# Kernel optimization log

Hardware: AMD Instinct MI355X
Metric: run time of the kernel (lower is better)

The kernel has to match this reference:

```python
import jax, jax.numpy as jnp
import numpy as np

B, T, C = 2, 2048, 1024
H = 16
D = C // H  # head_dim = 64


def setup_inputs() -> dict:
    key = jax.random.key(0)
    k1, k2, k3, k4, k5 = jax.random.split(key, 5)
    s = 0.02
    return {
        "x": jax.random.normal(k1, (B, T, C), dtype=jnp.float32),
        "w_qkv": jax.random.normal(k2, (C, 3 * C), dtype=jnp.float32) * s,
        "b_qkv": jnp.zeros((3 * C,), dtype=jnp.float32),
        "w_proj": jax.random.normal(k3, (C, C), dtype=jnp.float32) * s,
        "b_proj": jnp.zeros((C,), dtype=jnp.float32),
    }


def reference(x, w_qkv, b_qkv, w_proj, b_proj):
    b, t, c = x.shape
    qkv = x @ w_qkv + b_qkv                      # [B,T,3C]
    q, k, v = jnp.split(qkv, 3, axis=-1)
    # [B,T,C] -> [B,H,T,D]
    q = q.reshape(b, t, H, D).transpose(0, 2, 1, 3)
    k = k.reshape(b, t, H, D).transpose(0, 2, 1, 3)
    v = v.reshape(b, t, H, D).transpose(0, 2, 1, 3)
    att = jnp.einsum("bhqd,bhkd->bhqk", q, k) / jnp.sqrt(jnp.float32(D))
    causal = jnp.tril(jnp.ones((t, t), dtype=bool))  # True where allowed
    att = jnp.where(causal, att, -jnp.inf)
    att = jax.nn.softmax(att, axis=-1)
    out = jnp.einsum("bhqk,bhkd->bhqd", att, v)      # [B,H,T,D]
    out = out.transpose(0, 2, 1, 3).reshape(b, t, c)
    return out @ w_proj + b_proj
```

## Files before the change

### kernel.cpp

```cpp
#include <hip/hip_runtime.h>
#include <hip/hip_bf16.h>
#include <math.h>
#include <stdint.h>

#define B_ 2
#define T_ 2048
#define C_ 1024
#define H_ 16
#define D_ 64

typedef __attribute__((ext_vector_type(8))) short bf16x8;
typedef __attribute__((ext_vector_type(4))) float f32x4;

__device__ inline short f2bf(float f) {
  __hip_bfloat16 h = __float2bfloat16(f);
  return *(short*)&h;
}

__device__ inline void async16(const void* g, void* l) {
  __builtin_amdgcn_global_load_lds(
      (const __attribute__((address_space(1))) uint32_t*)g,
      (__attribute__((address_space(3))) uint32_t*)l, 16, 0, 0);
}


__global__ __launch_bounds__(256) void prep(
    const float* __restrict__ X, const float* __restrict__ Wq,
    const float* __restrict__ Wp, short* __restrict__ Xb,
    short* __restrict__ Wqt, short* __restrict__ Wpt) {
  const int tid = threadIdx.x;
  const int blk = blockIdx.x;
  __shared__ short Ts[64][68];

  if (blk < 512) {
    int t = blk * 256 + tid;
    int m = t >> 5, g = t & 31;
    const float* src = X + (size_t)m * C_ + g * 32;
    short* dst = Xb + (size_t)m * C_ + g * 32;
    int xv = (m >> 1) & 3;
    short out[32];
#pragma unroll
    for (int ch = 0; ch < 4; ++ch) {
      int sc = ch ^ xv;
#pragma unroll
      for (int e = 0; e < 8; e += 4) {
        float4 v = *(const float4*)(src + sc * 8 + e);
        out[ch * 8 + e + 0] = f2bf(v.x);
        out[ch * 8 + e + 1] = f2bf(v.y);
        out[ch * 8 + e + 2] = f2bf(v.z);
        out[ch * 8 + e + 3] = f2bf(v.w);
      }
    }
#pragma unroll
    for (int q = 0; q < 4; ++q) *(uint4*)(dst + q * 8) = *(uint4*)(out + q * 8);
    return;
  }

  const float* W;
  short* Wt;
  int N, n0, k0;
  if (blk < 1280) {
    int i = blk - 512;
    W = Wq; Wt = Wqt; N = 3 * C_;
    n0 = (i % 48) * 64; k0 = (i / 48) * 64;
  } else {
    int i = blk - 1280;
    W = Wp; Wt = Wpt; N = C_;
    n0 = (i & 15) * 64; k0 = (i >> 4) * 64;
  }
  {
    int r = tid >> 2, c0 = (tid & 3) * 16;
    const float* src = W + (size_t)(k0 + r) * N + n0 + c0;
#pragma unroll
    for (int u = 0; u < 16; u += 4) {
      float4 v = *(const float4*)(src + u);
      Ts[r][c0 + u + 0] = f2bf(v.x);
      Ts[r][c0 + u + 1] = f2bf(v.y);
      Ts[r][c0 + u + 2] = f2bf(v.z);
      Ts[r][c0 + u + 3] = f2bf(v.w);
    }
  }
  __syncthreads();
#pragma unroll
  for (int p = 0; p < 2; ++p) {
    int n = (tid >> 3) + p * 32;
    int kc = tid & 7;
    int xv = ((n0 + n) >> 1) & 3;
    int ka = kc * 8;
    int dk = (ka & ~31) | ((((ka >> 3) & 3) ^ xv) << 3);
    short tmp[8];
#pragma unroll
    for (int u = 0; u < 8; ++u) tmp[u] = Ts[ka + u][n];
    *(uint4*)(Wt + (size_t)(n0 + n) * 1024 + k0 + dk) = *(uint4*)tmp;
  }
}

template <int N, int BN, bool QKV>
__global__ __launch_bounds__(256) void gemm_mfma(
    const short* __restrict__ A, const short* __restrict__ Bt,
    const float* __restrict__ bias, short* __restrict__ Qp,
    short* __restrict__ Kp, short* __restrict__ Vp, float* __restrict__ Cout) {
  constexpr int NJ = BN / 32;
  constexpr int BI = BN * 32;
  const int tid = threadIdx.x;
  const int wave = tid >> 6, lane = tid & 63;
  const int quad = lane >> 4, l16 = lane & 15;
  const int wm = wave >> 1, wn = wave & 1;
  const int m0 = blockIdx.y * 128, n0 = blockIdx.x * BN;

  __shared__ short As[2][4096];
  __shared__ short Bs[2][BI];

  const int srow = tid >> 2, skc = tid & 3;
  const size_t arow0 = (size_t)(m0 + srow) * 1024 + skc * 8;
  const size_t brow0 = (size_t)(n0 + srow) * 1024 + skc * 8;

  f32x4 acc[4][NJ] = {};

  const int xi = quad ^ ((l16 >> 1) & 3);
  int aoff[4], boff[NJ];
#pragma unroll
  for (int i = 0; i < 4; ++i) aoff[i] = (wm * 64 + i * 16 + l16) * 32 + xi * 8;
#pragma unroll
  for (int j = 0; j < NJ; ++j)
    boff[j] = (wn * (BN / 2) + j * 16 + l16) * 32 + xi * 8;

  for (int k0 = 0; k0 < 1024; k0 += 64) {
    __syncthreads();
#pragma unroll
    for (int f = 0; f < 2; ++f) {
      const int kf = k0 + f * 32;
      async16(A + arow0 + kf, &As[f][tid * 8]);
      async16(A + arow0 + (size_t)64 * 1024 + kf, &As[f][2048 + tid * 8]);
      async16(Bt + brow0 + kf, &Bs[f][tid * 8]);
      if (BN == 128)
        async16(Bt + brow0 + (size_t)64 * 1024 + kf, &Bs[f][2048 + tid * 8]);
    }
    __syncthreads();

#pragma unroll
    for (int f = 0; f < 2; ++f) {
      bf16x8 af[4], bfr[NJ];
#pragma unroll
      for (int i = 0; i < 4; ++i) af[i] = *(const bf16x8*)&As[f][aoff[i]];
#pragma unroll
      for (int j = 0; j < NJ; ++j) bfr[j] = *(const bf16x8*)&Bs[f][boff[j]];
#pragma unroll
      for (int i = 0; i < 4; ++i)
#pragma unroll
        for (int j = 0; j < NJ; ++j)
          acc[i][j] = __builtin_amdgcn_mfma_f32_16x16x32_bf16(
              af[i], bfr[j], acc[i][j], 0, 0, 0);
    }
  }

  float bj[NJ];
#pragma unroll
  for (int j = 0; j < NJ; ++j) bj[j] = bias[n0 + wn * (BN / 2) + j * 16 + l16];

  if (QKV) {
#pragma unroll
    for (int i = 0; i < 4; ++i) {
#pragma unroll
      for (int reg = 0; reg < 4; ++reg) {
        int m = m0 + wm * 64 + i * 16 + quad * 4 + reg;
        int b = m >> 11, t = m & (T_ - 1);
#pragma unroll
        for (int j = 0; j < NJ; ++j) {
          int n = n0 + wn * (BN / 2) + j * 16 + l16;
          float v = acc[i][j][reg] + bj[j];
          int sel = n >> 10, cc = n & (C_ - 1);
          int hh = cc >> 6, d = cc & 63;
          size_t base = (size_t)(b * H_ + hh) * 131072 + (size_t)(t >> 6) * 4096;
          if (sel == 0) {
            Qp[base + (d >> 3) * 512 + (t & 63) * 8 + (d & 7)] = f2bf(v * 0.125f);
          } else if (sel == 1) {
            Kp[base + (d >> 3) * 512 + (t & 63) * 8 + (d & 7)] = f2bf(v);
          } else {
            Vp[base + ((t & 63) >> 3) * 512 + d * 8 + (t & 7)] = f2bf(v);
          }
        }
      }
    }
  } else {
#pragma unroll
    for (int i = 0; i < 4; ++i) {
#pragma unroll
      for (int reg = 0; reg < 4; ++reg) {
        int m = m0 + wm * 64 + i * 16 + quad * 4 + reg;
#pragma unroll
        for (int j = 0; j < NJ; ++j) {
          int n = n0 + wn * (BN / 2) + j * 16 + l16;
          Cout[(size_t)m * N + n] = acc[i][j][reg] + bj[j];
        }
      }
    }
  }
}

__global__ __launch_bounds__(256, 4) void attn_kernel(
    const short* __restrict__ Qt, const short* __restrict__ Kt,
    const short* __restrict__ Vt, short* __restrict__ attb) {
  const int tid = threadIdx.x;
  const int wave = tid >> 6, lane = tid & 63;
  const int quad = lane >> 4, l16 = lane & 15;

  const int blk = blockIdx.x;
  const int bh = (blk >> 5) & 31;
  const int k2 = blk >> 8;
  int qtt = ((blk & 31) + 8 * (k2 >> 1)) & 31;
  const int qt = (k2 & 1) ? (31 - qtt) : qtt;
  const int h = bh & 15, b = bh >> 4;
  const int q0 = qt * 64;

  const short* Qg = Qt + (size_t)bh * 131072;
  const short* Kg = Kt + (size_t)bh * 131072;
  const short* Vg = Vt + (size_t)bh * 131072;

  __shared__ short Ks[2][4096];
  __shared__ short Vs[2][4096];
  __shared__ short Ps[4096];

  const int rowl = 16 * wave + l16;

  bf16x8 bq[2];
#pragma unroll
  for (int f = 0; f < 2; ++f)
    bq[f] = *(const bf16x8*)(Qg + (size_t)(qt * 8 + 4 * f + quad) * 512 +
                             rowl * 8);

  async16(Kg + tid * 8, &Ks[0][tid * 8]);
  async16(Kg + 2048 + tid * 8, &Ks[0][2048 + tid * 8]);
  async16(Vg + tid * 8, &Vs[0][tid * 8]);
  async16(Vg + 2048 + tid * 8, &Vs[0][2048 + tid * 8]);

  f32x4 oacc[4] = {};
  float lsum = 0.f;

  for (int kt = 0; kt <= qt; ++kt) {
    const int buf = kt & 1;
    __syncthreads();
    if (kt < qt) {
      const short* kp = Kg + (size_t)(kt + 1) * 4096;
      const short* vp = Vg + (size_t)(kt + 1) * 4096;
      async16(kp + tid * 8, &Ks[buf ^ 1][tid * 8]);
      async16(kp + 2048 + tid * 8, &Ks[buf ^ 1][2048 + tid * 8]);
      async16(vp + tid * 8, &Vs[buf ^ 1][tid * 8]);
      async16(vp + 2048 + tid * 8, &Vs[buf ^ 1][2048 + tid * 8]);
    }

    f32x4 sacc[4] = {};
#pragma unroll
    for (int c = 0; c < 4; ++c) {
#pragma unroll
      for (int f = 0; f < 2; ++f) {
        bf16x8 ak = *(const bf16x8*)&Ks[buf][((4 * f + quad) * 64 + 16 * c + l16) * 8];
        sacc[c] = __builtin_amdgcn_mfma_f32_16x16x32_bf16(ak, bq[f], sacc[c], 0, 0, 0);
      }
    }

    const bool diag = (kt == qt);
#pragma unroll
    for (int c = 0; c < 4; ++c) {
      short4 pk;
#pragma unroll
      for (int reg = 0; reg < 4; ++reg) {
        int keyl = 16 * c + 4 * quad + reg;
        float p = (diag && keyl > rowl) ? 0.f : __expf(sacc[c][reg]);
        lsum += p;
        ((short*)&pk)[reg] = f2bf(p);
      }
      *(short4*)&Ps[(2 * c + (quad >> 1)) * 512 + rowl * 8 + (quad & 1) * 4] = pk;
    }

    __asm__ volatile("s_waitcnt lgkmcnt(0)" ::: "memory");

    bf16x8 ap[2];
#pragma unroll
    for (int f = 0; f < 2; ++f)
      ap[f] = *(const bf16x8*)&Ps[(4 * f + quad) * 512 + rowl * 8];
#pragma unroll
    for (int n = 0; n < 4; ++n) {
#pragma unroll
      for (int f = 0; f < 2; ++f) {
        bf16x8 bv = *(const bf16x8*)&Vs[buf][((4 * f + quad) * 64 + 16 * n + l16) * 8];
        oacc[n] = __builtin_amdgcn_mfma_f32_16x16x32_bf16(ap[f], bv, oacc[n], 0, 0, 0);
      }
    }
  }

  lsum += __shfl_xor(lsum, 16);
  lsum += __shfl_xor(lsum, 32);
  float linv[4];
#pragma unroll
  for (int reg = 0; reg < 4; ++reg)
    linv[reg] = 1.0f / __shfl(lsum, 4 * quad + reg, 64);

#pragma unroll
  for (int reg = 0; reg < 4; ++reg) {
    const int row = q0 + 16 * wave + 4 * quad + reg;
    const int m = b * T_ + row;
    const int xv = (m >> 1) & 3;
#pragma unroll
    for (int n = 0; n < 4; ++n) {
      int c = h * 64 + 16 * n + l16;
      int cs = (c & ~31) | ((((c >> 3) & 3) ^ xv) << 3) | (c & 7);
      attb[(size_t)m * C_ + cs] = f2bf(oacc[n][reg] * linv[reg]);
    }
  }
}

extern "C" void kernel_launch(void* const* d_in, const int* in_sizes, int n_in,
                              void* d_out, int out_size, void* d_ws, size_t ws_size,
                              hipStream_t stream) {
  const float* x      = (const float*)d_in[0];
  const float* w_qkv  = (const float*)d_in[1];
  const float* b_qkv  = (const float*)d_in[2];
  const float* w_proj = (const float*)d_in[3];
  const float* b_proj = (const float*)d_in[4];
  float* out = (float*)d_out;

  const size_t per = (size_t)B_ * H_ * T_ * D_;
  short* Qp   = (short*)d_ws;
  short* Kp   = Qp + per;
  short* Vp   = Kp + per;
  short* attb = Vp + per;
  short* xb   = attb + per;
  short* wqt  = xb + per;
  short* wpt  = wqt + (size_t)3 * C_ * C_;

  prep<<<1536, 256, 0, stream>>>(x, w_qkv, w_proj, xb, wqt, wpt);

  gemm_mfma<3 * C_, 128, true><<<dim3(24, 32), 256, 0, stream>>>(
      xb, wqt, b_qkv, Qp, Kp, Vp, nullptr);

  attn_kernel<<<dim3(1024), 256, 0, stream>>>(Qp, Kp, Vp, attb);

  gemm_mfma<C_, 64, false><<<dim3(16, 32), 256, 0, stream>>>(
      attb, wpt, b_proj, nullptr, nullptr, nullptr, out);
}
```

Before: 175.8 us.

## Enlarge attention query tile to 128 rows so each K/V tile serves two row groups

The attention kernel now handles 128 query rows per block: each wave owns two 16-row groups, and every K/V tile loaded into LDS feeds twice as many MFMAs. The grid is halved to 512 blocks with a new block-to-tile mapping that pairs light and heavy causal tiles. Waves whose query rows end before the last key tile skip compute on it but still join the barriers. Register pressure rises (launch bounds lowered to 3 waves per SIMD), and the causal imbalance inside a block leaves some waves idle.

Result: slower. 181.5 us (+3.2%).

```diff
diff --git a/kernel.cpp b/kernel.cpp
--- a/kernel.cpp
+++ b/kernel.cpp
@@ -198,7 +198,7 @@
   }
 }
 
-__global__ __launch_bounds__(256, 4) void attn_kernel(
+__global__ __launch_bounds__(256, 3) void attn_kernel(
     const short* __restrict__ Qt, const short* __restrict__ Kt,
     const short* __restrict__ Vt, short* __restrict__ attb) {
   const int tid = threadIdx.x;
@@ -206,12 +206,15 @@
   const int quad = lane >> 4, l16 = lane & 15;
 
   const int blk = blockIdx.x;
-  const int bh = (blk >> 5) & 31;
-  const int k2 = blk >> 8;
-  int qtt = ((blk & 31) + 8 * (k2 >> 1)) & 31;
-  const int qt = (k2 & 1) ? (31 - qtt) : qtt;
+  const int bh = blk & 31;
+  const int s3 = (blk >> 5) & 7;
+  const int qt = (blk & 256) ? (15 - s3) : s3;
   const int h = bh & 15, b = bh >> 4;
-  const int q0 = qt * 64;
+  const int q0 = qt * 128;
+
+  const int tq = 2 * qt + (wave >> 1);
+  const int KT = 2 * qt + 2;
+  const int rloc = 32 * (wave & 1) + l16;
 
   const short* Qg = Qt + (size_t)bh * 131072;
   const short* Kg = Kt + (size_t)bh * 131072;
@@ -219,28 +222,28 @@
 
   __shared__ short Ks[2][4096];
   __shared__ short Vs[2][4096];
-  __shared__ short Ps[4096];
-
-  const int rowl = 16 * wave + l16;
-
-  bf16x8 bq[2];
-#pragma unroll
-  for (int f = 0; f < 2; ++f)
-    bq[f] = *(const bf16x8*)(Qg + (size_t)(qt * 8 + 4 * f + quad) * 512 +
-                             rowl * 8);
+  __shared__ short Ps[8192];
+
+  bf16x8 bq[2][2];
+#pragma unroll
+  for (int rg = 0; rg < 2; ++rg)
+#pragma unroll
+    for (int f = 0; f < 2; ++f)
+      bq[rg][f] = *(const bf16x8*)(Qg + (size_t)(tq * 8 + 4 * f + quad) * 512 +
+                                   (rloc + 16 * rg) * 8);
 
   async16(Kg + tid * 8, &Ks[0][tid * 8]);
   async16(Kg + 2048 + tid * 8, &Ks[0][2048 + tid * 8]);
   async16(Vg + tid * 8, &Vs[0][tid * 8]);
   async16(Vg + 2048 + tid * 8, &Vs[0][2048 + tid * 8]);
 
-  f32x4 oacc[4] = {};
-  float lsum = 0.f;
-
-  for (int kt = 0; kt <= qt; ++kt) {
+  f32x4 oacc[2][4] = {};
+  float lsum[2] = {0.f, 0.f};
+
+  for (int kt = 0; kt < KT; ++kt) {
     const int buf = kt & 1;
     __syncthreads();
-    if (kt < qt) {
+    if (kt + 1 < KT) {
       const short* kp = Kg + (size_t)(kt + 1) * 4096;
       const short* vp = Vg + (size_t)(kt + 1) * 4096;
       async16(kp + tid * 8, &Ks[buf ^ 1][tid * 8]);
@@ -249,63 +252,82 @@
       async16(vp + 2048 + tid * 8, &Vs[buf ^ 1][2048 + tid * 8]);
     }
 
-    f32x4 sacc[4] = {};
-#pragma unroll
-    for (int c = 0; c < 4; ++c) {
-#pragma unroll
-      for (int f = 0; f < 2; ++f) {
-        bf16x8 ak = *(const bf16x8*)&Ks[buf][((4 * f + quad) * 64 + 16 * c + l16) * 8];
-        sacc[c] = __builtin_amdgcn_mfma_f32_16x16x32_bf16(ak, bq[f], sacc[c], 0, 0, 0);
-      }
-    }
-
-    const bool diag = (kt == qt);
-#pragma unroll
-    for (int c = 0; c < 4; ++c) {
-      short4 pk;
-#pragma unroll
-      for (int reg = 0; reg < 4; ++reg) {
-        int keyl = 16 * c + 4 * quad + reg;
-        float p = (diag && keyl > rowl) ? 0.f : __expf(sacc[c][reg]);
-        lsum += p;
-        ((short*)&pk)[reg] = f2bf(p);
-      }
-      *(short4*)&Ps[(2 * c + (quad >> 1)) * 512 + rowl * 8 + (quad & 1) * 4] = pk;
-    }
-
-    __asm__ volatile("s_waitcnt lgkmcnt(0)" ::: "memory");
-
-    bf16x8 ap[2];
-#pragma unroll
-    for (int f = 0; f < 2; ++f)
-      ap[f] = *(const bf16x8*)&Ps[(4 * f + quad) * 512 + rowl * 8];
-#pragma unroll
-    for (int n = 0; n < 4; ++n) {
-#pragma unroll
-      for (int f = 0; f < 2; ++f) {
-        bf16x8 bv = *(const bf16x8*)&Vs[buf][((4 * f + quad) * 64 + 16 * n + l16) * 8];
-        oacc[n] = __builtin_amdgcn_mfma_f32_16x16x32_bf16(ap[f], bv, oacc[n], 0, 0, 0);
-      }
-    }
-  }
-
-  lsum += __shfl_xor(lsum, 16);
-  lsum += __shfl_xor(lsum, 32);
-  float linv[4];
-#pragma unroll
-  for (int reg = 0; reg < 4; ++reg)
-    linv[reg] = 1.0f / __shfl(lsum, 4 * quad + reg, 64);
-
-#pragma unroll
-  for (int reg = 0; reg < 4; ++reg) {
-    const int row = q0 + 16 * wave + 4 * quad + reg;
-    const int m = b * T_ + row;
-    const int xv = (m >> 1) & 3;
-#pragma unroll
-    for (int n = 0; n < 4; ++n) {
-      int c = h * 64 + 16 * n + l16;
-      int cs = (c & ~31) | ((((c >> 3) & 3) ^ xv) << 3) | (c & 7);
-      attb[(size_t)m * C_ + cs] = f2bf(oacc[n][reg] * linv[reg]);
+    if (kt <= tq) {
+      f32x4 sacc[2][4] = {};
+#pragma unroll
+      for (int c = 0; c < 4; ++c) {
+#pragma unroll
+        for (int f = 0; f < 2; ++f) {
+          bf16x8 ak =
+              *(const bf16x8*)&Ks[buf][((4 * f + quad) * 64 + 16 * c + l16) * 8];
+#pragma unroll
+          for (int rg = 0; rg < 2; ++rg)
+            sacc[rg][c] = __builtin_amdgcn_mfma_f32_16x16x32_bf16(
+                ak, bq[rg][f], sacc[rg][c], 0, 0, 0);
+        }
+      }
+
+      const bool diag = (kt == tq);
+#pragma unroll
+      for (int rg = 0; rg < 2; ++rg) {
+        const int qloc = rloc + 16 * rg;
+        const int rs = 32 * wave + 16 * rg + l16;
+#pragma unroll
+        for (int c = 0; c < 4; ++c) {
+          short4 pk;
+#pragma unroll
+          for (int reg = 0; reg < 4; ++reg) {
+            int keyl = 16 * c + 4 * quad + reg;
+            float p = (diag && keyl > qloc) ? 0.f : __expf(sacc[rg][c][reg]);
+            lsum[rg] += p;
+            ((short*)&pk)[reg] = f2bf(p);
+          }
+          *(short4*)&Ps[(2 * c + (quad >> 1)) * 1024 + rs * 8 + (quad & 1) * 4] =
+              pk;
+        }
+      }
+
+      __asm__ volatile("s_waitcnt lgkmcnt(0)" ::: "memory");
+
+      bf16x8 ap[2][2];
+#pragma unroll
+      for (int rg = 0; rg < 2; ++rg)
+#pragma unroll
+        for (int f = 0; f < 2; ++f)
+          ap[rg][f] = *(const bf16x8*)&Ps[(4 * f + quad) * 1024 +
+                                          (32 * wave + 16 * rg + l16) * 8];
+#pragma unroll
+      for (int n = 0; n < 4; ++n) {
+#pragma unroll
+        for (int f = 0; f < 2; ++f) {
+          bf16x8 bv =
+              *(const bf16x8*)&Vs[buf][((4 * f + quad) * 64 + 16 * n + l16) * 8];
+#pragma unroll
+          for (int rg = 0; rg < 2; ++rg)
+            oacc[rg][n] = __builtin_amdgcn_mfma_f32_16x16x32_bf16(
+                ap[rg][f], bv, oacc[rg][n], 0, 0, 0);
+        }
+      }
+    }
+  }
+
+#pragma unroll
+  for (int rg = 0; rg < 2; ++rg) {
+    float ls = lsum[rg];
+    ls += __shfl_xor(ls, 16);
+    ls += __shfl_xor(ls, 32);
+#pragma unroll
+    for (int reg = 0; reg < 4; ++reg) {
+      const float linv = 1.0f / __shfl(ls, 4 * quad + reg, 64);
+      const int row = q0 + 32 * wave + 16 * rg + 4 * quad + reg;
+      const int m = b * T_ + row;
+      const int xv = (m >> 1) & 3;
+#pragma unroll
+      for (int n = 0; n < 4; ++n) {
+        int c = h * 64 + 16 * n + l16;
+        int cs = (c & ~31) | ((((c >> 3) & 3) ^ xv) << 3) | (c & 7);
+        attb[(size_t)m * C_ + cs] = f2bf(oacc[rg][n][reg] * linv);
+      }
     }
   }
 }
@@ -334,7 +356,7 @@
   gemm_mfma<3 * C_, 128, true><<<dim3(24, 32), 256, 0, stream>>>(
       xb, wqt, b_qkv, Qp, Kp, Vp, nullptr);
 
-  attn_kernel<<<dim3(1024), 256, 0, stream>>>(Qp, Kp, Vp, attb);
+  attn_kernel<<<dim3(512), 256, 0, stream>>>(Qp, Kp, Vp, attb);
 
   gemm_mfma<C_, 64, false><<<dim3(16, 32), 256, 0, stream>>>(
       attb, wpt, b_proj, nullptr, nullptr, nullptr, out);
```
